# Kernel tuning notes

Hardware: AMD Instinct MI355X
Metric: run time of the kernel (lower is better)

The kernel has to match this reference:

```python
import jax, jax.numpy as jnp
import numpy as np

N_NODES = 50000
IN_CH = 128
OUT_CH = 64
HID = 2 * OUT_CH  # 128
N_EDGES = 800000


def _glorot(key, shape):
    fan_in, fan_out = shape[0], shape[-1]
    lim = jnp.sqrt(6.0 / (fan_in + fan_out))
    return jax.random.uniform(key, shape, jnp.float32, -lim, lim)


def setup_inputs() -> dict:
    key = jax.random.key(0)
    ks = jax.random.split(key, 10)
    x = jax.random.normal(ks[0], (N_NODES, IN_CH), jnp.float32)
    edge_index = jax.random.randint(ks[1], (2, N_EDGES), 0, N_NODES, jnp.int32)
    return {
        "x": x,
        "edge_index": edge_index,
        "W1": _glorot(ks[2], (IN_CH, HID)),
        "a_src1": _glorot(ks[3], (HID,)),
        "a_dst1": _glorot(ks[4], (HID,)),
        "b1": jnp.zeros((HID,), jnp.float32),
        "W2": _glorot(ks[5], (HID, OUT_CH)),
        "a_src2": _glorot(ks[6], (OUT_CH,)),
        "a_dst2": _glorot(ks[7], (OUT_CH,)),
        "b2": jnp.zeros((OUT_CH,), jnp.float32),
    }


def _gat_conv(x, src, dst, W, a_src, a_dst, b, n_nodes):
    # Linear transform: [N, F_out]
    h = x @ W
    # Per-node attention halves (heads=1): alpha_i = <h_i, a>
    al_s = h @ a_src  # [N]
    al_d = h @ a_dst  # [N]
    # Edge scores with LeakyReLU(0.2), PyG default negative slope
    e = jax.nn.leaky_relu(al_s[src] + al_d[dst], negative_slope=0.2)
    # Segment softmax over incoming edges of each dst node
    m = jax.ops.segment_max(e, dst, num_segments=n_nodes)
    m = jnp.where(jnp.isfinite(m), m, 0.0)
    ex = jnp.exp(e - m[dst])
    denom = jax.ops.segment_sum(ex, dst, num_segments=n_nodes)
    alpha = ex / (denom[dst] + 1e-16)  # [E]
    # Weighted scatter-add aggregation
    out = jax.ops.segment_sum(h[src] * alpha[:, None], dst, num_segments=n_nodes)
    return out + b


def reference(x, edge_index, W1, a_src1, a_dst1, b1, W2, a_src2, a_dst2, b2):
    n = x.shape[0]
    # add_self_loops=True (PyG GATConv default)
    loops = jnp.arange(n, dtype=edge_index.dtype)
    src = jnp.concatenate([edge_index[0], loops])
    dst = jnp.concatenate([edge_index[1], loops])
    h = _gat_conv(x.astype(jnp.float32), src, dst, W1, a_src1, a_dst1, b1, n)
    h = jax.nn.relu(h)
    return _gat_conv(h, src, dst, W2, a_src2, a_dst2, b2, n)
```

## Files before the change

### kernel.cpp

```cpp
#include <hip/hip_runtime.h>
#include <hip/hip_bf16.h>

#define N_NODES 50000
#define IN_CH 128
#define HID 128
#define OUT_CH 64
#define N_EDGES 800000
#define N_TOT_EDGES (N_EDGES + N_NODES)
#define ET_PAD (N_TOT_EDGES + 3 * N_NODES)
#define MPAD 50048
#define NBN ((N_NODES + 255) / 256)
#define NB_ET ((N_TOT_EDGES + 255) / 256)
#define NB_GEMM (MPAD / 64)
#define NSH 128
#define EPS (N_EDGES / NSH)
#define NDW (N_NODES / 4)

typedef float float4v __attribute__((ext_vector_type(4)));
typedef unsigned uint4v __attribute__((ext_vector_type(4)));
typedef __attribute__((ext_vector_type(8))) short bf16x8;
typedef __attribute__((ext_vector_type(4))) float f32x4;

__device__ __forceinline__ unsigned bf16_rne(float f) {
    unsigned u = __float_as_uint(f);
    return (u + 0x7fffu + ((u >> 16) & 1u)) >> 16;
}
__device__ __forceinline__ unsigned pack2(float a, float b) {
    return bf16_rne(a) | (bf16_rne(b) << 16);
}

__global__ __launch_bounds__(256) void k_pre(
        const float* __restrict__ W1, unsigned short* __restrict__ Wl1,
        const float* __restrict__ W2, unsigned short* __restrict__ Wl2) {
    const int b = blockIdx.x, t = threadIdx.x;
    const float* W; unsigned short* Wl; int N, bb;
    if (b < 8) { W = W1; Wl = Wl1; N = 128; bb = b; }
    else       { W = W2; Wl = Wl2; N = 64;  bb = b - 8; }
    const int tg = bb * 256 + t;
    if (tg >= 16 * N) return;
    const int kg = tg / N, col = tg & (N - 1);
    float v[8];
    #pragma unroll
    for (int j = 0; j < 8; ++j) v[j] = W[(size_t)(kg * 8 + j) * N + col];
    uint4 p;
    p.x = pack2(v[0], v[1]); p.y = pack2(v[2], v[3]);
    p.z = pack2(v[4], v[5]); p.w = pack2(v[6], v[7]);
    *(uint4*)&Wl[(size_t)tg * 8] = p;
}

template<int N, bool AF32, bool USELDS>
__device__ __forceinline__ void gemm_body(int gb, int t,
        const float* __restrict__ Xf, const unsigned short* __restrict__ Xb,
        const unsigned short* __restrict__ Wlg,
        const float* __restrict__ asrc, const float* __restrict__ adst,
        unsigned short* __restrict__ Hb, float* __restrict__ als,
        float* __restrict__ ald, int M, unsigned short* Wl) {
    constexpr int NF = N / 16;
    const unsigned short* Wsrc;
    if constexpr (USELDS) {
        for (int i = t; i < N * 16; i += 256)
            ((uint4*)Wl)[i] = ((const uint4*)Wlg)[i];
        __syncthreads();
        Wsrc = Wl;
    } else {
        Wsrc = Wlg;
    }

    const int lane = t & 63, w = t >> 6;
    const int rb = gb * 64 + w * 16;
    const int cl = lane & 15, g = lane >> 4;

    f32x4 acc[NF];
    #pragma unroll
    for (int n = 0; n < NF; ++n) acc[n] = (f32x4){0.f, 0.f, 0.f, 0.f};

    const float* Xrow = nullptr;
    const unsigned short* Abase = nullptr;
    if constexpr (AF32) {
        const int arow = (rb + cl < M) ? (rb + cl) : (M - 1);
        Xrow = Xf + (size_t)arow * 128;
    } else {
        Abase = Xb + (size_t)(rb >> 4) * 2048 + cl * 8;
    }

    #pragma unroll
    for (int s = 0; s < 4; ++s) {
        bf16x8 af;
        if constexpr (AF32) {
            const int k0 = (s * 4 + g) * 8;
            float4 a = *(const float4*)&Xrow[k0];
            float4 c = *(const float4*)&Xrow[k0 + 4];
            uint4v uu;
            uu[0] = pack2(a.x, a.y); uu[1] = pack2(a.z, a.w);
            uu[2] = pack2(c.x, c.y); uu[3] = pack2(c.z, c.w);
            af = __builtin_bit_cast(bf16x8, uu);
        } else {
            af = *(const bf16x8*)(Abase + (s * 4 + g) * 128);
        }
        #pragma unroll
        for (int n = 0; n < NF; ++n) {
            bf16x8 bf = *(const bf16x8*)(Wsrc + ((s * 4 + g) * N + n * 16 + cl) * 8);
            acc[n] = __builtin_amdgcn_mfma_f32_16x16x32_bf16(af, bf, acc[n], 0, 0, 0);
        }
    }

    float asv[NF], adv[NF];
    #pragma unroll
    for (int n = 0; n < NF; ++n) {
        asv[n] = asrc[n * 16 + cl];
        adv[n] = adst[n * 16 + cl];
    }

    #pragma unroll
    for (int r = 0; r < 4; ++r) {
        float ps = 0.f, pd = 0.f;
        #pragma unroll
        for (int n = 0; n < NF; ++n) {
            ps += acc[n][r] * asv[n];
            pd += acc[n][r] * adv[n];
        }
        #pragma unroll
        for (int mask = 1; mask < 16; mask <<= 1) {
            ps += __shfl_xor(ps, mask);
            pd += __shfl_xor(pd, mask);
        }
        const int row = rb + g * 4 + r;
        if (cl == 0 && row < M) { als[row] = ps; ald[row] = pd; }
    }

    #pragma unroll
    for (int r = 0; r < 4; ++r) {
        const int row = rb + g * 4 + r;
        if (row >= M) continue;
        #pragma unroll
        for (int n = 0; n < NF; ++n)
            Hb[(size_t)(n >> 1) * (size_t)M * 32 + (size_t)row * 32
               + (n & 1) * 16 + cl] = (unsigned short)bf16_rne(acc[n][r]);
    }
}

__global__ __launch_bounds__(256) void k_par1(
        const int* __restrict__ ei, unsigned* __restrict__ cnt_s,
        unsigned char* __restrict__ rank8,
        const float* __restrict__ X, const unsigned short* __restrict__ Wl1,
        const float* __restrict__ asrc, const float* __restrict__ adst,
        unsigned short* __restrict__ Hb, float* __restrict__ als,
        float* __restrict__ ald, int M) {
    __shared__ unsigned lcnt[NDW];
    const int b = blockIdx.x, t = threadIdx.x;
    if (b < NSH) {
        const int s = b;
        for (int i = t; i < NDW; i += 256) lcnt[i] = 0;
        __syncthreads();
        const int base = s * EPS;
        const int* __restrict__ dst = ei + N_EDGES;
        for (int j = base + t; j < base + EPS; j += 256) {
            int d = __builtin_nontemporal_load(&dst[j]);
            unsigned sh = 8u * (d & 3);
            unsigned old = atomicAdd(&lcnt[d >> 2], 1u << sh);
            rank8[j] = (unsigned char)((old >> sh) & 0xFFu);
        }
        __syncthreads();
        unsigned* __restrict__ outp = cnt_s + (size_t)s * NDW;
        for (int i = t; i < NDW; i += 256) outp[i] = lcnt[i];
        return;
    }
    gemm_body<HID, true, false>(b - NSH, t, X, nullptr, Wl1,
                                asrc, adst, Hb, als, ald, M, nullptr);
}

__global__ void k_scan1(const unsigned* __restrict__ cnt_s, int* __restrict__ cntT,
                        unsigned char* __restrict__ pcoff8,
                        int* __restrict__ off, int* __restrict__ bsum, int n) {
    __shared__ int s[256];
    int t = threadIdx.x;
    int i = blockIdx.x * 256 + t;
    int padded = 0;
    if (i < n) {
        const int dw = i >> 2;
        const unsigned sh = 8u * (i & 3);
        int pc = 1;
        for (int c = 0; c < NSH; ++c) {
            pcoff8[(size_t)c * n + i] = (unsigned char)pc;
            pc += (int)((cnt_s[(size_t)c * NDW + dw] >> sh) & 0xFFu);
        }
        cntT[i] = pc;
        padded = (pc + 3) & ~3;
    }
    s[t] = padded;
    __syncthreads();
    for (int d = 1; d < 256; d <<= 1) {
        int x = (t >= d) ? s[t - d] : 0;
        __syncthreads();
        s[t] += x;
        __syncthreads();
    }
    if (i < n) off[i + 1] = s[t];
    if (t == 255) bsum[blockIdx.x] = s[255];
}

__global__ void k_scan3(int* __restrict__ off, const int* __restrict__ bsum, int n) {
    __shared__ int s[256];
    int t = threadIdx.x;
    s[t] = (t < NBN) ? bsum[t] : 0;
    __syncthreads();
    for (int d = 1; d < 256; d <<= 1) {
        int x = (t >= d) ? s[t - d] : 0;
        __syncthreads();
        s[t] += x;
        __syncthreads();
    }
    int base = (blockIdx.x > 0) ? s[blockIdx.x - 1] : 0;
    int i = blockIdx.x * 256 + t;
    if (i < n) off[i + 1] += base;
    if (i == 0) off[0] = 0;
}

__global__ void k_fillw(const int* __restrict__ ei, const int* __restrict__ off,
                        const unsigned char* __restrict__ rank8,
                        const unsigned char* __restrict__ pcoff8,
                        const float* __restrict__ als, const float* __restrict__ ald,
                        unsigned* __restrict__ ew, int e, int n) {
    int i = blockIdx.x * 256 + threadIdx.x;
    if (i < e) {
        int src = __builtin_nontemporal_load(&ei[i]);
        int dst = __builtin_nontemporal_load(&ei[e + i]);
        int c = i / EPS;
        int pos = off[dst] + (int)pcoff8[(size_t)c * n + dst] + (int)rank8[i];
        float ev = als[src] + ald[dst];
        ev = ev > 0.f ? ev : 0.2f * ev;
        ew[pos] = ((unsigned)src << 16) | bf16_rne(__expf(ev));
    } else if (i < e + n) {
        int v = i - e;
        float ev = als[v] + ald[v];
        ev = ev > 0.f ? ev : 0.2f * ev;
        ew[off[v]] = ((unsigned)v << 16) | bf16_rne(__expf(ev));
    }
}

__global__ __launch_bounds__(256) void k_inv(
        const int* __restrict__ off, const int* __restrict__ cntT,
        unsigned* __restrict__ ew, float* __restrict__ invden, int n) {
    const int fl = threadIdx.x & 15;
    const int v = blockIdx.x * 16 + (threadIdx.x >> 4);
    if (v >= n) return;
    const int start = off[v], end = start + cntT[v];
    const int pend = off[v + 1];
    float s = 0.f;
    for (int j = start + fl; j < end; j += 16)
        s += __uint_as_float(ew[j] << 16);
    for (int j = end + fl; j < pend; j += 16) ew[j] = 0;
    #pragma unroll
    for (int d = 1; d < 16; d <<= 1) s += __shfl_xor(s, d);
    if (fl == 0) invden[v] = 1.f / (s + 1e-16f);
}

__global__ __launch_bounds__(256) void gemm_mfma64(
        const unsigned short* __restrict__ Xb, const unsigned short* __restrict__ Wlg,
        const float* __restrict__ asrc, const float* __restrict__ adst,
        unsigned short* __restrict__ Hb, float* __restrict__ als,
        float* __restrict__ ald, int M) {
    __shared__ unsigned short Wl[16 * 64 * 8];
    gemm_body<OUT_CH, false, true>(blockIdx.x, threadIdx.x, nullptr, Xb, Wlg,
                                   asrc, adst, Hb, als, ald, M, Wl);
}

__global__ __launch_bounds__(256) void k_edgew2(
        const float* __restrict__ als, const float* __restrict__ ald,
        const int* __restrict__ off, const int* __restrict__ cntT,
        unsigned* __restrict__ ew, float* __restrict__ invden, int n) {
    const int fl = threadIdx.x & 15;
    const int v = blockIdx.x * 16 + (threadIdx.x >> 4);
    if (v >= n) return;
    const int start = off[v], end = start + cntT[v];
    const float aldv = ald[v];
    float s = 0.f;
    for (int j = start + fl; j < end; j += 16) {
        unsigned old = ew[j];
        int src = (int)(old >> 16);
        float e = als[src] + aldv;
        e = e > 0.f ? e : 0.2f * e;
        unsigned r = bf16_rne(__expf(e));
        ew[j] = (old & 0xFFFF0000u) | r;
        s += __uint_as_float(r << 16);
    }
    #pragma unroll
    for (int d = 1; d < 16; d <<= 1) s += __shfl_xor(s, d);
    if (fl == 0) invden[v] = 1.f / (s + 1e-16f);
}

template<int F, bool RELU, bool PACKOUT>
__global__ __launch_bounds__(256) void k_spmm_b(
        const unsigned short* __restrict__ Hb, const unsigned* __restrict__ ew,
        const float* __restrict__ invden, const float* __restrict__ bias,
        const int* __restrict__ off, void* __restrict__ outv, int n) {
    constexpr int NCH = F / 32;
    const int chunk = blockIdx.x % NCH;
    const int v = (blockIdx.x / NCH) * 64 + (threadIdx.x >> 2);
    if (v >= n) return;
    const int q = threadIdx.x & 3;
    const int start = off[v], end = off[v + 1];
    const unsigned short* __restrict__ Hch = Hb + (size_t)chunk * (size_t)n * 32 + q * 8;

    float a0[8] = {}, a1[8] = {}, a2[8] = {}, a3[8] = {};

    #define GATB(E, A)                                                   \
        {                                                                \
            float w_ = __uint_as_float((E) << 16);                       \
            uint4 h_ = *(const uint4*)&Hch[(size_t)((E) >> 16) * 32];    \
            A[0] += w_ * __uint_as_float(h_.x << 16);                    \
            A[1] += w_ * __uint_as_float(h_.x & 0xffff0000u);            \
            A[2] += w_ * __uint_as_float(h_.y << 16);                    \
            A[3] += w_ * __uint_as_float(h_.y & 0xffff0000u);            \
            A[4] += w_ * __uint_as_float(h_.z << 16);                    \
            A[5] += w_ * __uint_as_float(h_.z & 0xffff0000u);            \
            A[6] += w_ * __uint_as_float(h_.w << 16);                    \
            A[7] += w_ * __uint_as_float(h_.w & 0xffff0000u);            \
        }
    #define GATB4(Q) GATB((Q).x, a0) GATB((Q).y, a1) GATB((Q).z, a2) GATB((Q).w, a3)

    int j = start;
    for (; j + 4 < end; j += 8) {
        uint4 eA = *(const uint4*)&ew[j];
        uint4 eB = *(const uint4*)&ew[j + 4];
        GATB4(eA)
        GATB4(eB)
    }
    if (j < end) {
        uint4 eA = *(const uint4*)&ew[j];
        GATB4(eA)
    }
    #undef GATB4
    #undef GATB

    const float inv = invden[v];
    const float* __restrict__ bp = bias + chunk * 32 + q * 8;
    float s[8];
    #pragma unroll
    for (int i = 0; i < 8; ++i) {
        s[i] = (a0[i] + a1[i] + a2[i] + a3[i]) * inv + bp[i];
        if (RELU) s[i] = fmaxf(s[i], 0.f);
    }

    if (PACKOUT) {
        unsigned short* Xb2 = (unsigned short*)outv;
        const int kg = chunk * 4 + q;
        uint4v p;
        p[0] = pack2(s[0], s[1]); p[1] = pack2(s[2], s[3]);
        p[2] = pack2(s[4], s[5]); p[3] = pack2(s[6], s[7]);
        __builtin_nontemporal_store(p,
            (uint4v*)&Xb2[(size_t)(v >> 4) * 2048 + kg * 128 + (v & 15) * 8]);
    } else {
        float* out = (float*)outv;
        float4v o0, o1;
        o0[0] = s[0]; o0[1] = s[1]; o0[2] = s[2]; o0[3] = s[3];
        o1[0] = s[4]; o1[1] = s[5]; o1[2] = s[6]; o1[3] = s[7];
        float* op = out + (size_t)v * F + chunk * 32 + q * 8;
        __builtin_nontemporal_store(o0, (float4v*)op);
        __builtin_nontemporal_store(o1, (float4v*)(op + 4));
    }
}


extern "C" void kernel_launch(void* const* d_in, const int* in_sizes, int n_in,
                              void* d_out, int out_size, void* d_ws, size_t ws_size,
                              hipStream_t stream) {
    const float* x     = (const float*)d_in[0];
    const int*   ei    = (const int*)d_in[1];
    const float* W1    = (const float*)d_in[2];
    const float* as1   = (const float*)d_in[3];
    const float* ad1   = (const float*)d_in[4];
    const float* b1    = (const float*)d_in[5];
    const float* W2    = (const float*)d_in[6];
    const float* as2   = (const float*)d_in[7];
    const float* ad2   = (const float*)d_in[8];
    const float* b2    = (const float*)d_in[9];
    float* out = (float*)d_out;

    const int Nn = N_NODES;

    char* ws = (char*)d_ws;
    size_t o = 0;
    auto carve = [&](size_t bytes) { char* p = ws + o; o = (o + bytes + 255) & ~(size_t)255; return p; };
    int*            off   = (int*)carve((Nn + 1) * sizeof(int));
    int*            cntT  = (int*)carve(Nn * sizeof(int));
    int*            bsum  = (int*)carve(256 * sizeof(int));
    unsigned char*  rank8 = (unsigned char*)carve((size_t)N_EDGES);
    unsigned*       cnt_s = (unsigned*)carve((size_t)NSH * NDW * sizeof(unsigned));
    unsigned char*  pcoff8= (unsigned char*)carve((size_t)NSH * Nn);
    unsigned*       ew    = (unsigned*)carve((size_t)ET_PAD * sizeof(unsigned));
    unsigned short* h1b   = (unsigned short*)carve((size_t)Nn * HID * sizeof(unsigned short));
    unsigned short* h2b   = (unsigned short*)carve((size_t)Nn * OUT_CH * sizeof(unsigned short));
    unsigned short* Xb2   = (unsigned short*)carve((size_t)MPAD * 128 * sizeof(unsigned short));
    unsigned short* Wl1   = (unsigned short*)carve(16 * 128 * 8 * sizeof(unsigned short));
    unsigned short* Wl2   = (unsigned short*)carve(16 * 64 * 8 * sizeof(unsigned short));
    float*          als   = (float*)carve(Nn * sizeof(float));
    float*          ald   = (float*)carve(Nn * sizeof(float));
    float*          invd  = (float*)carve(Nn * sizeof(float));

    k_pre<<<12, 256, 0, stream>>>(W1, Wl1, W2, Wl2);

    k_par1<<<NSH + NB_GEMM, 256, 0, stream>>>(
        ei, cnt_s, rank8, x, Wl1, as1, ad1, h1b, als, ald, Nn);

    k_scan1<<<NBN, 256, 0, stream>>>(cnt_s, cntT, pcoff8, off, bsum, Nn);
    k_scan3<<<NBN, 256, 0, stream>>>(off, bsum, Nn);

    k_fillw<<<NB_ET, 256, 0, stream>>>(ei, off, rank8, pcoff8, als, ald,
                                       ew, N_EDGES, Nn);

    const int nbEW  = (Nn + 15) / 16;
    const int nbN64 = (Nn + 63) / 64;

    k_inv<<<nbEW, 256, 0, stream>>>(off, cntT, ew, invd, Nn);

    k_spmm_b<HID, true, true><<<nbN64 * (HID / 32), 256, 0, stream>>>(
        h1b, ew, invd, b1, off, Xb2, Nn);

    gemm_mfma64<<<NB_GEMM, 256, 0, stream>>>(
        Xb2, Wl2, as2, ad2, h2b, als, ald, Nn);
    k_edgew2<<<nbEW, 256, 0, stream>>>(als, ald, off, cntT, ew, invd, Nn);
    k_spmm_b<OUT_CH, false, false><<<nbN64 * (OUT_CH / 32), 256, 0, stream>>>(
        h2b, ew, invd, b2, off, out, Nn);
}
```

Baseline: 147.9 us.

## Fuse softmax denominator and layer-2 edge weights into the SpMM kernels

Removes the separate k_inv and k_edgew2 passes. Each SpMM thread now accumulates the softmax denominator itself and masks padded slots by index, instead of relying on a pass that zeroed them. The layer-2 SpMM computes the exp edge weights inline from the second layer's attention logits, which now live in separate buffers. This saves two kernel launches and two full passes over the edge array. The cost is redundant exp and als gathers across feature chunks and lanes. Padded entries are no longer zeroed, so garbage source indices are still gathered, and a NaN there would survive the zero weight.

Result: faster. 142.2 us (-3.9%).

```diff
diff --git a/kernel.cpp b/kernel.cpp
--- a/kernel.cpp
+++ b/kernel.cpp
@@ -238,23 +238,6 @@
     }
 }
 
-__global__ __launch_bounds__(256) void k_inv(
-        const int* __restrict__ off, const int* __restrict__ cntT,
-        unsigned* __restrict__ ew, float* __restrict__ invden, int n) {
-    const int fl = threadIdx.x & 15;
-    const int v = blockIdx.x * 16 + (threadIdx.x >> 4);
-    if (v >= n) return;
-    const int start = off[v], end = start + cntT[v];
-    const int pend = off[v + 1];
-    float s = 0.f;
-    for (int j = start + fl; j < end; j += 16)
-        s += __uint_as_float(ew[j] << 16);
-    for (int j = end + fl; j < pend; j += 16) ew[j] = 0;
-    #pragma unroll
-    for (int d = 1; d < 16; d <<= 1) s += __shfl_xor(s, d);
-    if (fl == 0) invden[v] = 1.f / (s + 1e-16f);
-}
-
 __global__ __launch_bounds__(256) void gemm_mfma64(
         const unsigned short* __restrict__ Xb, const unsigned short* __restrict__ Wlg,
         const float* __restrict__ asrc, const float* __restrict__ adst,
@@ -265,48 +248,38 @@
                                    asrc, adst, Hb, als, ald, M, Wl);
 }
 
-__global__ __launch_bounds__(256) void k_edgew2(
-        const float* __restrict__ als, const float* __restrict__ ald,
-        const int* __restrict__ off, const int* __restrict__ cntT,
-        unsigned* __restrict__ ew, float* __restrict__ invden, int n) {
-    const int fl = threadIdx.x & 15;
-    const int v = blockIdx.x * 16 + (threadIdx.x >> 4);
-    if (v >= n) return;
-    const int start = off[v], end = start + cntT[v];
-    const float aldv = ald[v];
-    float s = 0.f;
-    for (int j = start + fl; j < end; j += 16) {
-        unsigned old = ew[j];
-        int src = (int)(old >> 16);
-        float e = als[src] + aldv;
-        e = e > 0.f ? e : 0.2f * e;
-        unsigned r = bf16_rne(__expf(e));
-        ew[j] = (old & 0xFFFF0000u) | r;
-        s += __uint_as_float(r << 16);
-    }
-    #pragma unroll
-    for (int d = 1; d < 16; d <<= 1) s += __shfl_xor(s, d);
-    if (fl == 0) invden[v] = 1.f / (s + 1e-16f);
-}
-
-template<int F, bool RELU, bool PACKOUT>
+template<int F, bool RELU, bool PACKOUT, bool INLINEW>
 __global__ __launch_bounds__(256) void k_spmm_b(
         const unsigned short* __restrict__ Hb, const unsigned* __restrict__ ew,
-        const float* __restrict__ invden, const float* __restrict__ bias,
-        const int* __restrict__ off, void* __restrict__ outv, int n) {
+        const float* __restrict__ als, const float* __restrict__ ald,
+        const float* __restrict__ bias, const int* __restrict__ off,
+        const int* __restrict__ cntT, void* __restrict__ outv, int n) {
     constexpr int NCH = F / 32;
     const int chunk = blockIdx.x % NCH;
     const int v = (blockIdx.x / NCH) * 64 + (threadIdx.x >> 2);
     if (v >= n) return;
     const int q = threadIdx.x & 3;
-    const int start = off[v], end = off[v + 1];
+    const int start = off[v], pend = off[v + 1];
+    const int rend = start + cntT[v];
+    const float aldv = INLINEW ? ald[v] : 0.f;
     const unsigned short* __restrict__ Hch = Hb + (size_t)chunk * (size_t)n * 32 + q * 8;
 
     float a0[8] = {}, a1[8] = {}, a2[8] = {}, a3[8] = {};
-
-    #define GATB(E, A)                                                   \
+    float denom = 0.f;
+
+    #define GATB(E, A, IDX)                                              \
         {                                                                \
-            float w_ = __uint_as_float((E) << 16);                       \
+            float w_;                                                    \
+            if (INLINEW) {                                               \
+                int s_ = (int)((E) >> 16);                               \
+                float e_ = als[s_] + aldv;                               \
+                e_ = e_ > 0.f ? e_ : 0.2f * e_;                          \
+                w_ = __expf(e_);                                         \
+            } else {                                                     \
+                w_ = __uint_as_float((E) << 16);                         \
+            }                                                            \
+            w_ = ((IDX) < rend) ? w_ : 0.f;                              \
+            denom += w_;                                                 \
             uint4 h_ = *(const uint4*)&Hch[(size_t)((E) >> 16) * 32];    \
             A[0] += w_ * __uint_as_float(h_.x << 16);                    \
             A[1] += w_ * __uint_as_float(h_.x & 0xffff0000u);            \
@@ -317,23 +290,24 @@
             A[6] += w_ * __uint_as_float(h_.w << 16);                    \
             A[7] += w_ * __uint_as_float(h_.w & 0xffff0000u);            \
         }
-    #define GATB4(Q) GATB((Q).x, a0) GATB((Q).y, a1) GATB((Q).z, a2) GATB((Q).w, a3)
+    #define GATB4(Q, J) GATB((Q).x, a0, (J)) GATB((Q).y, a1, (J)+1) \
+                        GATB((Q).z, a2, (J)+2) GATB((Q).w, a3, (J)+3)
 
     int j = start;
-    for (; j + 4 < end; j += 8) {
+    for (; j + 4 < pend; j += 8) {
         uint4 eA = *(const uint4*)&ew[j];
         uint4 eB = *(const uint4*)&ew[j + 4];
-        GATB4(eA)
-        GATB4(eB)
-    }
-    if (j < end) {
+        GATB4(eA, j)
+        GATB4(eB, j + 4)
+    }
+    if (j < pend) {
         uint4 eA = *(const uint4*)&ew[j];
-        GATB4(eA)
+        GATB4(eA, j)
     }
     #undef GATB4
     #undef GATB
 
-    const float inv = invden[v];
+    const float inv = 1.f / (denom + 1e-16f);
     const float* __restrict__ bp = bias + chunk * 32 + q * 8;
     float s[8];
     #pragma unroll
@@ -394,32 +368,30 @@
     unsigned short* Xb2   = (unsigned short*)carve((size_t)MPAD * 128 * sizeof(unsigned short));
     unsigned short* Wl1   = (unsigned short*)carve(16 * 128 * 8 * sizeof(unsigned short));
     unsigned short* Wl2   = (unsigned short*)carve(16 * 64 * 8 * sizeof(unsigned short));
-    float*          als   = (float*)carve(Nn * sizeof(float));
-    float*          ald   = (float*)carve(Nn * sizeof(float));
-    float*          invd  = (float*)carve(Nn * sizeof(float));
+    float*          als1v = (float*)carve(Nn * sizeof(float));
+    float*          ald1v = (float*)carve(Nn * sizeof(float));
+    float*          als2v = (float*)carve(Nn * sizeof(float));
+    float*          ald2v = (float*)carve(Nn * sizeof(float));
 
     k_pre<<<12, 256, 0, stream>>>(W1, Wl1, W2, Wl2);
 
     k_par1<<<NSH + NB_GEMM, 256, 0, stream>>>(
-        ei, cnt_s, rank8, x, Wl1, as1, ad1, h1b, als, ald, Nn);
+        ei, cnt_s, rank8, x, Wl1, as1, ad1, h1b, als1v, ald1v, Nn);
 
     k_scan1<<<NBN, 256, 0, stream>>>(cnt_s, cntT, pcoff8, off, bsum, Nn);
     k_scan3<<<NBN, 256, 0, stream>>>(off, bsum, Nn);
 
-    k_fillw<<<NB_ET, 256, 0, stream>>>(ei, off, rank8, pcoff8, als, ald,
+    k_fillw<<<NB_ET, 256, 0, stream>>>(ei, off, rank8, pcoff8, als1v, ald1v,
                                        ew, N_EDGES, Nn);
 
-    const int nbEW  = (Nn + 15) / 16;
     const int nbN64 = (Nn + 63) / 64;
 
-    k_inv<<<nbEW, 256, 0, stream>>>(off, cntT, ew, invd, Nn);
-
-    k_spmm_b<HID, true, true><<<nbN64 * (HID / 32), 256, 0, stream>>>(
-        h1b, ew, invd, b1, off, Xb2, Nn);
+    k_spmm_b<HID, true, true, false><<<nbN64 * (HID / 32), 256, 0, stream>>>(
+        h1b, ew, nullptr, nullptr, b1, off, cntT, Xb2, Nn);
 
     gemm_mfma64<<<NB_GEMM, 256, 0, stream>>>(
-        Xb2, Wl2, as2, ad2, h2b, als, ald, Nn);
-    k_edgew2<<<nbEW, 256, 0, stream>>>(als, ald, off, cntT, ew, invd, Nn);
-    k_spmm_b<OUT_CH, false, false><<<nbN64 * (OUT_CH / 32), 256, 0, stream>>>(
-        h2b, ew, invd, b2, off, out, Nn);
-}
+        Xb2, Wl2, as2, ad2, h2b, als2v, ald2v, Nn);
+
+    k_spmm_b<OUT_CH, false, false, true><<<nbN64 * (OUT_CH / 32), 256, 0, stream>>>(
+        h2b, ew, als2v, ald2v, b2, off, cntT, out, Nn);
+}
```
